# Kernel optimization log

Hardware: AMD Instinct MI355X
Metric: run time of the kernel (lower is better)

Reference implementation:

```python
import jax, jax.numpy as jnp
import numpy as np

N = 50000
E = 500000
IN_C = 100
HID = 80
OUT = 80
EDGE_DIM = 100
NUM_AGGR = 6
NUM_SCALE = 5

# PNA degree statistics, computed from the degree histogram exactly as PyG does
DEG_HIST = np.array([240, 328, 79, 39, 23, 12, 11, 7, 6, 5, 7, 3, 1, 0, 2, 0, 0, 0, 1], dtype=np.float64)
_bins = np.arange(len(DEG_HIST), dtype=np.float64)
_tot = DEG_HIST.sum()
AVG_LIN = np.float32((_bins * DEG_HIST).sum() / _tot)
AVG_LOG = np.float32((np.log(_bins + 1.0) * DEG_HIST).sum() / _tot)


def _lin_init(key, fan_in, fan_out):
    k1, k2 = jax.random.split(key)
    bound = 1.0 / np.sqrt(fan_in)
    W = jax.random.uniform(k1, (fan_in, fan_out), minval=-bound, maxval=bound, dtype=jnp.float32)
    b = jax.random.uniform(k2, (fan_out,), minval=-bound, maxval=bound, dtype=jnp.float32)
    return W, b


def setup_inputs() -> dict:
    key = jax.random.key(0)
    ks = jax.random.split(key, 20)
    inp = {}
    inp["x1"] = jax.random.normal(ks[0], (N, IN_C), jnp.float32)
    inp["edge_index1"] = jax.random.randint(ks[1], (2, E), 0, N)
    inp["edge_attr1"] = jax.random.normal(ks[2], (E, EDGE_DIM), jnp.float32)
    inp["x2"] = jax.random.normal(ks[3], (N, IN_C), jnp.float32)
    inp["edge_index2"] = jax.random.randint(ks[4], (2, E), 0, N)
    inp["edge_attr2"] = jax.random.normal(ks[5], (E, EDGE_DIM), jnp.float32)
    # conv1 params (F_in=100 -> F_out=80)
    inp["We1"], inp["be1"] = _lin_init(ks[6], EDGE_DIM, IN_C)
    inp["Wpre1"], inp["bpre1"] = _lin_init(ks[7], 3 * IN_C, IN_C)
    inp["Wpost1"], inp["bpost1"] = _lin_init(ks[8], (NUM_AGGR * NUM_SCALE + 1) * IN_C, HID)
    inp["Wlin1"], inp["blin1"] = _lin_init(ks[9], HID, HID)
    # conv2 params (F_in=80 -> F_out=80)
    inp["We2"], inp["be2"] = _lin_init(ks[10], EDGE_DIM, HID)
    inp["Wpre2"], inp["bpre2"] = _lin_init(ks[11], 3 * HID, HID)
    inp["Wpost2"], inp["bpost2"] = _lin_init(ks[12], (NUM_AGGR * NUM_SCALE + 1) * HID, OUT)
    inp["Wlin2"], inp["blin2"] = _lin_init(ks[13], OUT, OUT)
    # MLP head
    inp["Wfc1"], inp["bfc1"] = _lin_init(ks[14], OUT, 80)
    inp["Wfc2"], inp["bfc2"] = _lin_init(ks[15], 80, OUT)
    return inp


def _pna(x, src, dst, edge_attr, We, be, Wpre, bpre, Wpost, bpost, Wlin, blin):
    """PNAConv, towers=1, pre_layers=1, post_layers=1, divide_input=False."""
    F_in = x.shape[1]
    e = edge_attr @ We + be                                    # [E, F] edge encoder
    # pre_nn(cat([x_i, x_j, e])) done as 3 matmuls to avoid [E, 3F] concat
    W_i, W_j, W_e = Wpre[:F_in], Wpre[F_in:2 * F_in], Wpre[2 * F_in:]
    h = x[dst] @ W_i + x[src] @ W_j + e @ W_e + bpre           # [E, F] messages
    cnt = jax.ops.segment_sum(jnp.ones((h.shape[0],), h.dtype), dst, N)  # in-degree
    deg = jnp.maximum(cnt, 1.0)
    s = jax.ops.segment_sum(h, dst, N)                         # sum aggr
    mean = s / deg[:, None]
    mean_sq = jax.ops.segment_sum(h * h, dst, N) / deg[:, None]
    var = mean_sq - mean * mean
    std = jnp.sqrt(jnp.maximum(var, 0.0) + 1e-5)
    has = (cnt > 0)[:, None]
    mn = jnp.where(has, jax.ops.segment_min(h, dst, N), 0.0)
    mx = jnp.where(has, jax.ops.segment_max(h, dst, N), 0.0)
    agg = jnp.concatenate([s, mean, mn, mx, var, std], axis=-1)  # [N, 6F]
    logd = jnp.log(deg + 1.0)
    scaled = jnp.concatenate([
        agg,
        agg * (logd / AVG_LOG)[:, None],     # amplification
        agg * (AVG_LOG / logd)[:, None],     # attenuation
        agg * (deg / AVG_LIN)[:, None],      # linear
        agg * (AVG_LIN / deg)[:, None],      # inverse_linear
    ], axis=-1)                              # [N, 30F]
    out = jnp.concatenate([x, scaled], axis=-1) @ Wpost + bpost  # post_nn
    return out @ Wlin + blin


def _branch(x, edge_index, edge_attr, c1, c2, Wfc1, bfc1, Wfc2, bfc2):
    src, dst = edge_index[0], edge_index[1]
    x = jax.nn.relu(_pna(x, src, dst, edge_attr, *c1))
    x = _pna(x, src, dst, edge_attr, *c2)
    x = jax.nn.relu(x @ Wfc1 + bfc1)
    return x @ Wfc2 + bfc2


def reference(x1, edge_index1, edge_attr1, x2, edge_index2, edge_attr2,
              We1, be1, Wpre1, bpre1, Wpost1, bpost1, Wlin1, blin1,
              We2, be2, Wpre2, bpre2, Wpost2, bpost2, Wlin2, blin2,
              Wfc1, bfc1, Wfc2, bfc2):
    c1 = (We1, be1, Wpre1, bpre1, Wpost1, bpost1, Wlin1, blin1)
    c2 = (We2, be2, Wpre2, bpre2, Wpost2, bpost2, Wlin2, blin2)
    out1 = _branch(x1, edge_index1, edge_attr1, c1, c2, Wfc1, bfc1, Wfc2, bfc2)
    out2 = _branch(x2, edge_index2, edge_attr2, c1, c2, Wfc1, bfc1, Wfc2, bfc2)
    return (out1, out2)
```

## Files before the change

### kernel.cpp

```cpp
#include <hip/hip_runtime.h>
#include <cmath>

static constexpr int NN = 50000;
static constexpr int EE = 500000;

typedef short v8s __attribute__((ext_vector_type(8)));
typedef float v4f __attribute__((ext_vector_type(4)));

__device__ inline short f2bf(float x){
  union{float f; unsigned u;} v{x};
  unsigned r = v.u + 0x7fffu + ((v.u >> 16) & 1u);
  return (short)(r >> 16);
}
__device__ inline float b2f(short s){
  union{unsigned u; float f;} v; v.u = ((unsigned)(unsigned short)s) << 16; return v.f;
}


__global__ __launch_bounds__(256)
void count_deg_k(const int* __restrict__ dst, int* __restrict__ cnt, int e_total){
  int e = blockIdx.x*256 + threadIdx.x;
  if (e < e_total) atomicAdd(&cnt[dst[e]], 1);
}

__global__ __launch_bounds__(1024)
void scan_block_k(const int* __restrict__ cnt, int* __restrict__ pre,
                  int* __restrict__ bsum, int n){
  __shared__ int tmp[1024];
  int b = blockIdx.x, t = threadIdx.x, i = b*1024 + t;
  int v = (i < n) ? cnt[i] : 0;
  tmp[t] = v; __syncthreads();
  for (int off = 1; off < 1024; off <<= 1){
    int u = (t >= off) ? tmp[t-off] : 0;
    __syncthreads();
    tmp[t] += u;
    __syncthreads();
  }
  if (i < n) pre[i] = tmp[t];
  if (t == 1023) bsum[b] = tmp[t];
}

__global__ void scan_sums_k(int* __restrict__ bsum, int nb){
  if (threadIdx.x == 0){
    int s = 0;
    for (int i = 0; i < nb; i++){ int v = bsum[i]; bsum[i] = s; s += v; }
  }
}

__global__ __launch_bounds__(256)
void scan_finalize_k(const int* __restrict__ pre, const int* __restrict__ bsum,
                     int* __restrict__ offs, int n){
  int i = blockIdx.x*256 + threadIdx.x;
  if (i < n) offs[i+1] = pre[i] + bsum[i >> 10];
  if (i == 0) offs[0] = 0;
}

__global__ __launch_bounds__(256)
void fill_csr_k(const int* __restrict__ dst, const int* __restrict__ src,
                const int* __restrict__ offs, int* __restrict__ cursor,
                int* __restrict__ eids, int* __restrict__ srcs_csr, int e_total){
  int e = blockIdx.x*256 + threadIdx.x;
  if (e < e_total){
    int d = dst[e];
    int p = offs[d] + atomicAdd(&cursor[d], 1);
    eids[p] = e;
    srcs_csr[p] = src[e];
  }
}


__global__ __launch_bounds__(128)
void vecmat_bias_k(const float* __restrict__ v, const float* __restrict__ B,
                   const float* __restrict__ b2, float* __restrict__ out, int K, int Nc){
  int c = blockIdx.x*128 + threadIdx.x;
  if (c < Nc){
    float s = b2[c];
    for (int k = 0; k < K; k++) s += v[k]*B[(size_t)k*Nc + c];
    out[c] = s;
  }
}

__global__ __launch_bounds__(256)
void sgemm_k(const float* __restrict__ A, const float* __restrict__ B,
             float* __restrict__ C, int M, int K, int Nc){
  __shared__ float As[16][65];
  __shared__ float Bs[16][65];
  int bm = blockIdx.x*64, bn = blockIdx.y*64;
  int tid = threadIdx.x;
  int tx = tid & 15, ty = tid >> 4;
  float acc[4][4] = {};
  for (int k0 = 0; k0 < K; k0 += 16){
    #pragma unroll
    for (int i = 0; i < 4; i++){
      int t = tid + 256*i;
      int r = t >> 4, c = t & 15;
      int gr = bm + r, gc = k0 + c;
      As[c][r] = (gr < M && gc < K) ? A[(size_t)gr*K + gc] : 0.f;
    }
    #pragma unroll
    for (int i = 0; i < 4; i++){
      int t = tid + 256*i;
      int r = t >> 6, c = t & 63;
      int gr = k0 + r, gc = bn + c;
      Bs[r][c] = (gr < K && gc < Nc) ? B[(size_t)gr*Nc + gc] : 0.f;
    }
    __syncthreads();
    #pragma unroll
    for (int kk = 0; kk < 16; kk++){
      float a[4], b[4];
      #pragma unroll
      for (int i = 0; i < 4; i++) a[i] = As[kk][ty*4 + i];
      #pragma unroll
      for (int j = 0; j < 4; j++) b[j] = Bs[kk][tx*4 + j];
      #pragma unroll
      for (int i = 0; i < 4; i++)
        #pragma unroll
        for (int j = 0; j < 4; j++) acc[i][j] += a[i]*b[j];
    }
    __syncthreads();
  }
  #pragma unroll
  for (int i = 0; i < 4; i++){
    int gr = bm + ty*4 + i;
    if (gr >= M) continue;
    #pragma unroll
    for (int j = 0; j < 4; j++){
      int gc = bn + tx*4 + j;
      if (gc < Nc) C[(size_t)gr*Nc + gc] = acc[i][j];
    }
  }
}

__global__ __launch_bounds__(256)
void tconv_k(const float* __restrict__ src, int K, int ldsrc, int Ncols,
             short* __restrict__ dst, int Kpad){
  int c = blockIdx.x;
  int k = blockIdx.y*256 + threadIdx.x;
  if (c < Ncols && k < Kpad)
    dst[(long)c*Kpad + k] = (k < K) ? f2bf(src[(long)k*ldsrc + c]) : (short)0;
}

__global__ __launch_bounds__(256)
void btpost_k(const float* __restrict__ Wpost, int F, int Kpad,
              short* __restrict__ dst){
  int cp = blockIdx.x;
  int k = blockIdx.y*256 + threadIdx.x;
  if (k >= Kpad) return;
  int g = cp / 80, c = cp - g*80;
  float v = 0.f;
  if (k < F){ if (g == 0) v = Wpost[(long)k*80 + c]; }
  else if (k < 7*F) v = Wpost[(long)(F + g*6*F + (k - F))*80 + c];
  dst[(long)cp*Kpad + k] = f2bf(v);
}

__global__ __launch_bounds__(256)
void cvt_rows_k(const float* __restrict__ src, int K, short* __restrict__ dst,
                int ldd, long total){
  long i = (long)blockIdx.x*256 + threadIdx.x;
  if (i >= total) return;
  int n = (int)(i / K), c = (int)(i - (long)n*K);
  dst[(long)n*ldd + c] = f2bf(src[i]);
}

template<int NFR, bool A_F32, bool C_F32, bool RELU>
__global__ __launch_bounds__(512)
void egemm_k(const void* __restrict__ Av, long lda, int Kreal,
             const short* __restrict__ Bt, const float* __restrict__ bias,
             void* __restrict__ Cv, long ldc, int M, int ncols, int wlim)
{
  constexpr int BN = NFR*16;
  constexpr int PITCH = BN + 8;
  constexpr int NCH = 2*NFR;
  __shared__ short Bs[BN][136];
  __shared__ short stage[8*8*PITCH];
  const float* Af = (const float*)Av;
  const short* Ab = (const short*)Av;
  short* Cb = (short*)Cv;
  float* Cf = (float*)Cv;

  int bn = blockIdx.y*BN;
  for (int u = threadIdx.x; u < BN*16; u += 512){
    int c = u >> 4, k8 = (u & 15)*8;
    v8s vv = (v8s)0;
    if (bn + c < ncols) vv = *(const v8s*)(Bt + (long)(bn + c)*128 + k8);
    *(v8s*)&Bs[c][k8] = vv;
  }
  __syncthreads();

  int lane = threadIdx.x & 63;
  int lr = lane & 15, lkg = lane >> 4;
  int w = threadIdx.x >> 6;
  short* st = stage + w*8*PITCH;
  int w0 = (blockIdx.x*512 + threadIdx.x) >> 6;
  int nw = gridDim.x * 8;
  int Mtiles = (M + 31) >> 5;

  float bvs[NFR];
  #pragma unroll
  for (int n = 0; n < NFR; n++) bvs[n] = bias ? bias[bn + n*16 + lr] : 0.f;

  for (int t = w0; t < Mtiles; t += nw){
    int base = t*32;
    long r0 = base + lr;      if (r0 > M-1) r0 = M-1;
    long r1 = base + 16 + lr; if (r1 > M-1) r1 = M-1;

    v8s a0[4], a1[4];
    if constexpr (A_F32){
      const float* p0 = Af + r0*lda;
      const float* p1 = Af + r1*lda;
      #pragma unroll
      for (int ks = 0; ks < 4; ks++){
        int kb = ks*32 + lkg*8;
        v8s o0 = (v8s)0, o1 = (v8s)0;
        if (kb + 3 < Kreal){
          float4 f0 = *(const float4*)(p0 + kb);
          float4 f1 = *(const float4*)(p1 + kb);
          o0[0]=f2bf(f0.x); o0[1]=f2bf(f0.y); o0[2]=f2bf(f0.z); o0[3]=f2bf(f0.w);
          o1[0]=f2bf(f1.x); o1[1]=f2bf(f1.y); o1[2]=f2bf(f1.z); o1[3]=f2bf(f1.w);
        }
        if (kb + 7 < Kreal){
          float4 f0 = *(const float4*)(p0 + kb + 4);
          float4 f1 = *(const float4*)(p1 + kb + 4);
          o0[4]=f2bf(f0.x); o0[5]=f2bf(f0.y); o0[6]=f2bf(f0.z); o0[7]=f2bf(f0.w);
          o1[4]=f2bf(f1.x); o1[5]=f2bf(f1.y); o1[6]=f2bf(f1.z); o1[7]=f2bf(f1.w);
        }
        a0[ks] = o0; a1[ks] = o1;
      }
    } else {
      const short* p0 = Ab + r0*lda + lkg*8;
      const short* p1 = Ab + r1*lda + lkg*8;
      #pragma unroll
      for (int ks = 0; ks < 4; ks++){
        a0[ks] = *(const v8s*)(p0 + ks*32);
        a1[ks] = *(const v8s*)(p1 + ks*32);
      }
    }

    v4f acc0[NFR], acc1[NFR];
    #pragma unroll
    for (int n = 0; n < NFR; n++){ acc0[n] = (v4f)0.f; acc1[n] = (v4f)0.f; }
    #pragma unroll
    for (int ks = 0; ks < 4; ks++){
      #pragma unroll
      for (int n = 0; n < NFR; n++){
        v8s b = *(const v8s*)&Bs[n*16 + lr][ks*32 + lkg*8];
        acc0[n] = __builtin_amdgcn_mfma_f32_16x16x32_bf16(a0[ks], b, acc0[n], 0, 0, 0);
        acc1[n] = __builtin_amdgcn_mfma_f32_16x16x32_bf16(a1[ks], b, acc1[n], 0, 0, 0);
      }
    }

    if constexpr (C_F32){
      #pragma unroll
      for (int n = 0; n < NFR; n++){
        int col = bn + n*16 + lr;
        if (col >= ncols) continue;
        #pragma unroll
        for (int j = 0; j < 4; j++){
          int row = base + lkg*4 + j;
          float v0 = acc0[n][j] + bvs[n];
          float v1 = acc1[n][j] + bvs[n];
          if (RELU){ v0 = fmaxf(v0, 0.f); v1 = fmaxf(v1, 0.f); }
          if (row < M)      Cf[(long)row*ldc + col] = v0;
          if (row + 16 < M) Cf[(long)(row+16)*ldc + col] = v1;
        }
      }
    } else {
      #pragma unroll
      for (int q = 0; q < 4; q++){
        if ((lkg >> 1) == (q & 1)){
          int srow = (lkg & 1)*4;
          #pragma unroll
          for (int n = 0; n < NFR; n++){
            #pragma unroll
            for (int j = 0; j < 4; j++){
              float v = ((q < 2) ? acc0[n][j] : acc1[n][j]) + bvs[n];
              if (RELU) v = fmaxf(v, 0.f);
              st[(srow + j)*PITCH + n*16 + lr] = f2bf(v);
            }
          }
        }
        int rb = base + q*8;
        #pragma unroll
        for (int i = 0; i < (8*NCH + 63)/64; i++){
          int c = i*64 + lane;
          if (c < 8*NCH){
            int r = c/NCH, off8 = (c - r*NCH)*8;
            int grow = rb + r;
            if (grow < M && off8 < wlim - (bn & 0))
              if (bn + off8 < wlim)
                *(v8s*)(Cb + (long)grow*ldc + bn + off8) = *(const v8s*)&st[r*PITCH + off8];
          }
        }
      }
    }
  }
}

__global__ __launch_bounds__(512)
void pgemm_k(const short* __restrict__ Ab, int kpad,
             const short* __restrict__ Bt, const float* __restrict__ scl,
             const float* __restrict__ bias, short* __restrict__ C, int M)
{
  __shared__ short Bs[400][40];
  __shared__ short AsSt[10240];
  short (*As)[40] = (short(*)[40])AsSt;

  int tid = threadIdx.x;
  int w = tid >> 6, lane = tid & 63;
  int lr = lane & 15, lkg = lane >> 4;
  int bm = blockIdx.x*128;

  v4f acc[25];
  #pragma unroll
  for (int n = 0; n < 25; n++) acc[n] = (v4f)0.f;

  for (int k0 = 0; k0 < kpad; k0 += 32){
    {
      int u = tid;
      int r = u >> 2, c8 = (u & 3)*8;
      int grow = bm + r;
      v8s out = (v8s)0;
      if (grow < M) out = *(const v8s*)(Ab + (long)grow*kpad + k0 + c8);
      *(v8s*)&As[r][c8] = out;
    }
    for (int u = tid; u < 400*4; u += 512){
      int c = u >> 2, k8 = (u & 3)*8;
      *(v8s*)&Bs[c][k8] = *(const v8s*)(Bt + (long)c*kpad + k0 + k8);
    }
    __syncthreads();
    {
      v8s a = *(const v8s*)&As[w*16 + lr][lkg*8];
      #pragma unroll
      for (int n = 0; n < 25; n++){
        v8s b = *(const v8s*)&Bs[n*16 + lr][lkg*8];
        acc[n] = __builtin_amdgcn_mfma_f32_16x16x32_bf16(a, b, acc[n], 0, 0, 0);
      }
    }
    __syncthreads();
  }

  short* st = AsSt + w*16*80;
  float sc[4][5];
  #pragma unroll
  for (int j = 0; j < 4; j++){
    int row = bm + w*16 + lkg*4 + j;
    int rr = row < M ? row : 0;
    #pragma unroll
    for (int g = 0; g < 5; g++) sc[j][g] = scl[rr*5 + g];
  }
  #pragma unroll
  for (int cc = 0; cc < 5; cc++){
    float bv = bias[cc*16 + lr];
    #pragma unroll
    for (int j = 0; j < 4; j++){
      float v = bv;
      #pragma unroll
      for (int g = 0; g < 5; g++) v += sc[j][g]*acc[5*g + cc][j];
      st[(lkg*4 + j)*80 + cc*16 + lr] = f2bf(v);
    }
  }
  #pragma unroll
  for (int i = 0; i < 3; i++){
    int c = i*64 + lane;
    if (c < 160){
      int r = c/10, off = (c - r*10)*8;
      int grow = bm + w*16 + r;
      if (grow < M)
        *(v8s*)(C + (long)grow*128 + off) = *(const v8s*)&st[r*80 + off];
    }
  }
}

template<int F>
__global__ __launch_bounds__(256)
void aggregate_k(const short* __restrict__ xixj, int ldx,
                 const short* __restrict__ epc, int epoff,
                 const int* __restrict__ eids,
                 const int* __restrict__ offs, const int* __restrict__ srcs_csr,
                 short* __restrict__ aggout, long ldk,
                 float* __restrict__ scl, float avg_lin, float avg_log, int n){
  int wnode = (blockIdx.x*256 + threadIdx.x) >> 6;
  int lane = threadIdx.x & 63;
  if (wnode >= n) return;
  constexpr int C2 = F - 64;
  int beg = offs[wnode], end = offs[wnode+1];
  float xi0 = b2f(xixj[(long)wnode*ldx + lane]);
  float xi1 = (lane < C2) ? b2f(xixj[(long)wnode*ldx + 64 + lane]) : 0.f;
  float s0 = 0.f, q0 = 0.f, mn0 = INFINITY, mx0 = -INFINITY;
  float s1 = 0.f, q1 = 0.f, mn1 = INFINITY, mx1 = -INFINITY;
  for (int p = beg; p < end; p++){
    int s = srcs_csr[p];
    long e = eids[p];
    float h0 = xi0 + b2f(xixj[(long)s*ldx + F + lane]) + b2f(epc[e*192 + epoff + lane]);
    s0 += h0; q0 += h0*h0; mn0 = fminf(mn0, h0); mx0 = fmaxf(mx0, h0);
    if (lane < C2){
      float h1 = xi1 + b2f(xixj[(long)s*ldx + F + 64 + lane]) + b2f(epc[e*192 + epoff + 64 + lane]);
      s1 += h1; q1 += h1*h1; mn1 = fminf(mn1, h1); mx1 = fmaxf(mx1, h1);
    }
  }
  int cnt = end - beg;
  float deg = (float)(cnt > 1 ? cnt : 1);
  if (cnt == 0){ mn0 = 0.f; mx0 = 0.f; mn1 = 0.f; mx1 = 0.f; }
  float mean0 = s0/deg, var0 = q0/deg - mean0*mean0;
  float std0 = sqrtf(fmaxf(var0, 0.f) + 1e-5f);
  short* a = aggout + (long)wnode*ldk;
  a[lane] = f2bf(s0); a[F+lane] = f2bf(mean0); a[2*F+lane] = f2bf(mn0);
  a[3*F+lane] = f2bf(mx0); a[4*F+lane] = f2bf(var0); a[5*F+lane] = f2bf(std0);
  if (lane < C2){
    float mean1 = s1/deg, var1 = q1/deg - mean1*mean1;
    float std1 = sqrtf(fmaxf(var1, 0.f) + 1e-5f);
    int l2 = 64 + lane;
    a[l2] = f2bf(s1); a[F+l2] = f2bf(mean1); a[2*F+l2] = f2bf(mn1);
    a[3*F+l2] = f2bf(mx1); a[4*F+l2] = f2bf(var1); a[5*F+l2] = f2bf(std1);
  }
  if (lane == 0){
    float logd = logf(deg + 1.f);
    scl[wnode*5+0] = 1.f;
    scl[wnode*5+1] = logd/avg_log;
    scl[wnode*5+2] = avg_log/logd;
    scl[wnode*5+3] = deg/avg_lin;
    scl[wnode*5+4] = avg_lin/deg;
  }
}


extern "C" void kernel_launch(void* const* d_in, const int* in_sizes, int n_in,
                              void* d_out, int out_size, void* d_ws, size_t ws_size,
                              hipStream_t stream){
  const float* x1   = (const float*)d_in[0];
  const int*   ei1  = (const int*)  d_in[1];
  const float* ea1  = (const float*)d_in[2];
  const float* x2   = (const float*)d_in[3];
  const int*   ei2  = (const int*)  d_in[4];
  const float* ea2  = (const float*)d_in[5];
  const float* We1  = (const float*)d_in[6],  *be1   = (const float*)d_in[7];
  const float* Wpre1= (const float*)d_in[8],  *bpre1 = (const float*)d_in[9];
  const float* Wpost1=(const float*)d_in[10], *bpost1= (const float*)d_in[11];
  const float* Wlin1= (const float*)d_in[12], *blin1 = (const float*)d_in[13];
  const float* We2  = (const float*)d_in[14], *be2   = (const float*)d_in[15];
  const float* Wpre2= (const float*)d_in[16], *bpre2 = (const float*)d_in[17];
  const float* Wpost2=(const float*)d_in[18], *bpost2= (const float*)d_in[19];
  const float* Wlin2= (const float*)d_in[20], *blin2 = (const float*)d_in[21];
  const float* Wfc1 = (const float*)d_in[22], *bfc1  = (const float*)d_in[23];
  const float* Wfc2 = (const float*)d_in[24], *bfc2  = (const float*)d_in[25];

  static const double HIST[19] = {240,328,79,39,23,12,11,7,6,5,7,3,1,0,2,0,0,0,1};
  double tot = 0, lin = 0, lg = 0;
  for (int i = 0; i < 19; i++){ tot += HIST[i]; lin += i*HIST[i]; lg += log((double)i + 1.0)*HIST[i]; }
  float avg_lin = (float)(lin/tot), avg_log = (float)(lg/tot);

  const int KP1 = 704, KP2 = 576;

  uintptr_t pw = (uintptr_t)d_ws;
  auto carve = [&](size_t b)->void*{ void* r = (void*)pw; pw += (b + 255) & ~(size_t)255; return r; };
  int*   cnt      = (int*)  carve((size_t)NN*4);
  int*   pre      = (int*)  carve((size_t)NN*4);
  int*   bsum     = (int*)  carve(64*4);
  int*   offs     = (int*)  carve((size_t)(NN+1)*4);
  int*   cursor   = (int*)  carve((size_t)NN*4);
  int*   eids     = (int*)  carve((size_t)EE*4);
  int*   srcs_csr = (int*)  carve((size_t)EE*4);
  float* WecA     = (float*)carve(100*100*4);
  float* WecB     = (float*)carve(100*80*4);
  float* Wlf      = (float*)carve(80*80*4);
  float* becf     = (float*)carve(256*4);
  float* blf      = (float*)carve(128*4);
  short* Btep12   = (short*)carve((size_t)192*128*2);
  short* Btij1    = (short*)carve((size_t)208*128*2);
  short* Btij2    = (short*)carve((size_t)160*128*2);
  short* Btpost1  = (short*)carve((size_t)400*KP1*2);
  short* Btpost2  = (short*)carve((size_t)400*KP2*2);
  short* Btlin1   = (short*)carve((size_t)80*128*2);
  short* Btlf     = (short*)carve((size_t)80*128*2);
  short* Btfc2    = (short*)carve((size_t)80*128*2);
  short* Aprime1  = (short*)carve((size_t)NN*KP1*2);
  short* Aprime2  = (short*)carve((size_t)NN*KP2*2);
  short* xixjb    = (short*)carve((size_t)NN*224*2);
  short* epc      = (short*)carve((size_t)EE*192*2);
  float* scl      = (float*)carve((size_t)NN*5*4);
  short* tpost    = (short*)carve((size_t)NN*128*2);
  short* tD       = (short*)carve((size_t)NN*128*2);

  dim3 blk(256);
  const int NB = (NN + 1023)/1024;
  const int NTILES = (NN + 31)/32;
  const int GB_N  = (NTILES + 7)/8;
  const int GB_E  = 341;

  sgemm_k<<<dim3(2,2), blk, 0, stream>>>(We1, Wpre1 + 2*100*100, WecA, 100, 100, 100);
  sgemm_k<<<dim3(2,2), blk, 0, stream>>>(We2, Wpre2 + 2*80*80,  WecB, 100, 80, 80);
  sgemm_k<<<dim3(2,2), blk, 0, stream>>>(Wlin2, Wfc1, Wlf, 80, 80, 80);
  hipMemsetAsync(becf, 0, 256*4, stream);
  vecmat_bias_k<<<dim3(1), dim3(128), 0, stream>>>(be1, Wpre1 + 2*100*100, bpre1, becf, 100, 100);
  vecmat_bias_k<<<dim3(1), dim3(128), 0, stream>>>(be2, Wpre2 + 2*80*80,  bpre2, becf + 100, 80, 80);
  vecmat_bias_k<<<dim3(1), dim3(128), 0, stream>>>(blin2, Wfc1, bfc1, blf, 80, 80);
  tconv_k<<<dim3(100,1), blk, 0, stream>>>(WecA, 100, 100, 100, Btep12, 128);
  tconv_k<<<dim3(80,1),  blk, 0, stream>>>(WecB, 100,  80,  80, Btep12 + 100*128, 128);
  hipMemsetAsync(Btep12 + 180*128, 0, (size_t)12*128*2, stream);
  tconv_k<<<dim3(100,1), blk, 0, stream>>>(Wpre1,           100, 100, 100, Btij1,           128);
  tconv_k<<<dim3(100,1), blk, 0, stream>>>(Wpre1 + 100*100, 100, 100, 100, Btij1 + 100*128, 128);
  hipMemsetAsync(Btij1 + 200*128, 0, (size_t)8*128*2, stream);
  tconv_k<<<dim3(80,1),  blk, 0, stream>>>(Wpre2,           80, 80, 80, Btij2,          128);
  tconv_k<<<dim3(80,1),  blk, 0, stream>>>(Wpre2 + 80*80,   80, 80, 80, Btij2 + 80*128, 128);
  btpost_k<<<dim3(400,(KP1+255)/256), blk, 0, stream>>>(Wpost1, 100, KP1, Btpost1);
  btpost_k<<<dim3(400,(KP2+255)/256), blk, 0, stream>>>(Wpost2,  80, KP2, Btpost2);
  tconv_k<<<dim3(80,1), blk, 0, stream>>>(Wlin1, 80, 80, 80, Btlin1, 128);
  tconv_k<<<dim3(80,1), blk, 0, stream>>>(Wlf,   80, 80, 80, Btlf,   128);
  tconv_k<<<dim3(80,1), blk, 0, stream>>>(Wfc2,  80, 80, 80, Btfc2,  128);
  hipMemsetAsync(Aprime1, 0, (size_t)NN*KP1*2, stream);
  hipMemsetAsync(Aprime2, 0, (size_t)NN*KP2*2, stream);
  hipMemsetAsync(tpost,   0, (size_t)NN*128*2, stream);
  hipMemsetAsync(tD,      0, (size_t)NN*128*2, stream);

  for (int b = 0; b < 2; b++){
    const float* x  = b ? x2  : x1;
    const int*   ei = b ? ei2 : ei1;
    const float* ea = b ? ea2 : ea1;
    float* outb = (float*)d_out + (size_t)b*NN*80;
    const int* src = ei;
    const int* dst = ei + EE;

    hipMemsetAsync(cnt, 0, (size_t)NN*4, stream);
    hipMemsetAsync(cursor, 0, (size_t)NN*4, stream);
    count_deg_k<<<dim3((EE+255)/256), blk, 0, stream>>>(dst, cnt, EE);
    scan_block_k<<<dim3(NB), dim3(1024), 0, stream>>>(cnt, pre, bsum, NN);
    scan_sums_k<<<dim3(1), dim3(64), 0, stream>>>(bsum, NB);
    scan_finalize_k<<<dim3((NN+255)/256), blk, 0, stream>>>(pre, bsum, offs, NN);
    fill_csr_k<<<dim3((EE+255)/256), blk, 0, stream>>>(dst, src, offs, cursor, eids, srcs_csr, EE);

    egemm_k<4,true,false,false><<<dim3(GB_E,3), dim3(512), 0, stream>>>(
        ea, 100, 100, Btep12, becf, epc, 192, EE, 180, 192);

    cvt_rows_k<<<dim3((int)(((long)NN*100 + 255)/256)), blk, 0, stream>>>(x, 100, Aprime1, KP1, (long)NN*100);

    egemm_k<5,false,false,false><<<dim3(GB_N,3), dim3(512), 0, stream>>>(
        Aprime1, KP1, 0, Btij1, nullptr, xixjb, 224, NN, 200, 200);
    aggregate_k<100><<<dim3((NN+3)/4), blk, 0, stream>>>(
        xixjb, 224, epc, 0, eids, offs, srcs_csr, Aprime1 + 100, KP1, scl, avg_lin, avg_log, NN);
    pgemm_k<<<dim3((NN+127)/128), dim3(512), 0, stream>>>(
        Aprime1, KP1, Btpost1, scl, bpost1, tpost, NN);
    egemm_k<5,false,false,true><<<dim3(GB_N,1), dim3(512), 0, stream>>>(
        tpost, 128, 0, Btlin1, blin1, Aprime2, KP2, NN, 80, 80);

    egemm_k<5,false,false,false><<<dim3(GB_N,2), dim3(512), 0, stream>>>(
        Aprime2, KP2, 0, Btij2, nullptr, xixjb, 160, NN, 160, 160);
    aggregate_k<80><<<dim3((NN+3)/4), blk, 0, stream>>>(
        xixjb, 160, epc, 100, eids, offs, srcs_csr, Aprime2 + 80, KP2, scl, avg_lin, avg_log, NN);
    pgemm_k<<<dim3((NN+127)/128), dim3(512), 0, stream>>>(
        Aprime2, KP2, Btpost2, scl, bpost2, tpost, NN);

    egemm_k<5,false,false,true><<<dim3(GB_N,1), dim3(512), 0, stream>>>(
        tpost, 128, 0, Btlf, blf, tD, 128, NN, 80, 80);
    egemm_k<5,false,true,false><<<dim3(GB_N,1), dim3(512), 0, stream>>>(
        tD, 128, 0, Btfc2, bfc2, outb, 80, NN, 80, 80);
  }
}
```

Measured before the change: 1.497 ms.

## Batch setup kernels, pack CSR edges, shrink GEMM blocks, use packed bf16 convert

Several small prep launches (vecmat, tconv, memsets) are merged into multi-job kernels, and the full-buffer memsets become a pad-only zeroing kernel. The CSR edge id and source arrays are packed into one int2 array, so aggregation does a single load per edge. egemm blocks drop from 512 to 256 threads with new grid sizes, and the edge GEMM moves to 6 fragments over 2 column blocks. The fp32 A path loads all values first and converts them with the hardware packed bf16 instruction. The goal is less launch overhead and better memory-level parallelism, at the cost of possible occupancy and rounding-behaviour differences.

Result: faster. 1.322 ms (-11.7%).

```diff
diff --git a/kernel.cpp b/kernel.cpp
--- a/kernel.cpp
+++ b/kernel.cpp
@@ -14,6 +14,11 @@
 }
 __device__ inline float b2f(short s){
   union{unsigned u; float f;} v; v.u = ((unsigned)(unsigned short)s) << 16; return v.f;
+}
+__device__ inline unsigned cvtpk(float lo, float hi){
+  unsigned r;
+  asm("v_cvt_pk_bf16_f32 %0, %1, %2" : "=v"(r) : "v"(lo), "v"(hi));
+  return r;
 }
 
 
@@ -58,25 +63,26 @@
 __global__ __launch_bounds__(256)
 void fill_csr_k(const int* __restrict__ dst, const int* __restrict__ src,
                 const int* __restrict__ offs, int* __restrict__ cursor,
-                int* __restrict__ eids, int* __restrict__ srcs_csr, int e_total){
+                int2* __restrict__ edg, int e_total){
   int e = blockIdx.x*256 + threadIdx.x;
   if (e < e_total){
     int d = dst[e];
     int p = offs[d] + atomicAdd(&cursor[d], 1);
-    eids[p] = e;
-    srcs_csr[p] = src[e];
-  }
-}
-
-
+    edg[p] = make_int2(e, src[e]);
+  }
+}
+
+
+struct VJob { const float* v; const float* B; const float* b2; float* out; int K, Nc; };
+struct VJobs { VJob j[3]; };
 __global__ __launch_bounds__(128)
-void vecmat_bias_k(const float* __restrict__ v, const float* __restrict__ B,
-                   const float* __restrict__ b2, float* __restrict__ out, int K, int Nc){
-  int c = blockIdx.x*128 + threadIdx.x;
-  if (c < Nc){
-    float s = b2[c];
-    for (int k = 0; k < K; k++) s += v[k]*B[(size_t)k*Nc + c];
-    out[c] = s;
+void vecmat_multi_k(VJobs js){
+  const VJob J = js.j[blockIdx.y];
+  int c = threadIdx.x;
+  if (c < J.Nc){
+    float s = J.b2[c];
+    for (int k = 0; k < J.K; k++) s += J.v[k]*J.B[(size_t)k*J.Nc + c];
+    J.out[c] = s;
   }
 }
 
@@ -131,13 +137,15 @@
   }
 }
 
-__global__ __launch_bounds__(256)
-void tconv_k(const float* __restrict__ src, int K, int ldsrc, int Ncols,
-             short* __restrict__ dst, int Kpad){
+struct TJob { const float* src; short* dst; int K, ldsrc, Ncols; };
+struct TJobs { TJob j[9]; };
+__global__ __launch_bounds__(128)
+void tconv_multi_k(TJobs js){
+  const TJob J = js.j[blockIdx.y];
   int c = blockIdx.x;
-  int k = blockIdx.y*256 + threadIdx.x;
-  if (c < Ncols && k < Kpad)
-    dst[(long)c*Kpad + k] = (k < K) ? f2bf(src[(long)k*ldsrc + c]) : (short)0;
+  int k = threadIdx.x;
+  if (c < J.Ncols)
+    J.dst[(long)c*128 + k] = (k < J.K) ? f2bf(J.src[(long)k*J.ldsrc + c]) : (short)0;
 }
 
 __global__ __launch_bounds__(256)
@@ -162,8 +170,18 @@
   dst[(long)n*ldd + c] = f2bf(src[i]);
 }
 
+struct ZJob { short* p; int ld, c0, nc, rows; };
+struct ZJobs { ZJob j[4]; };
+__global__ __launch_bounds__(256)
+void zeropad_k(ZJobs js){
+  const ZJob J = js.j[blockIdx.y];
+  int i = blockIdx.x*256 + threadIdx.x;
+  int r = i / J.nc, c = i - r*J.nc;
+  if (r < J.rows) J.p[(long)r*J.ld + J.c0 + c] = 0;
+}
+
 template<int NFR, bool A_F32, bool C_F32, bool RELU>
-__global__ __launch_bounds__(512)
+__global__ __launch_bounds__(256)
 void egemm_k(const void* __restrict__ Av, long lda, int Kreal,
              const short* __restrict__ Bt, const float* __restrict__ bias,
              void* __restrict__ Cv, long ldc, int M, int ncols, int wlim)
@@ -172,14 +190,14 @@
   constexpr int PITCH = BN + 8;
   constexpr int NCH = 2*NFR;
   __shared__ short Bs[BN][136];
-  __shared__ short stage[8*8*PITCH];
+  __shared__ short stage[4*8*PITCH];
   const float* Af = (const float*)Av;
   const short* Ab = (const short*)Av;
   short* Cb = (short*)Cv;
   float* Cf = (float*)Cv;
 
   int bn = blockIdx.y*BN;
-  for (int u = threadIdx.x; u < BN*16; u += 512){
+  for (int u = threadIdx.x; u < BN*16; u += 256){
     int c = u >> 4, k8 = (u & 15)*8;
     v8s vv = (v8s)0;
     if (bn + c < ncols) vv = *(const v8s*)(Bt + (long)(bn + c)*128 + k8);
@@ -191,8 +209,8 @@
   int lr = lane & 15, lkg = lane >> 4;
   int w = threadIdx.x >> 6;
   short* st = stage + w*8*PITCH;
-  int w0 = (blockIdx.x*512 + threadIdx.x) >> 6;
-  int nw = gridDim.x * 8;
+  int w0 = (blockIdx.x*256 + threadIdx.x) >> 6;
+  int nw = gridDim.x * 4;
   int Mtiles = (M + 31) >> 5;
 
   float bvs[NFR];
@@ -208,23 +226,28 @@
     if constexpr (A_F32){
       const float* p0 = Af + r0*lda;
       const float* p1 = Af + r1*lda;
+      float4 f0[8], f1[8];
       #pragma unroll
       for (int ks = 0; ks < 4; ks++){
         int kb = ks*32 + lkg*8;
-        v8s o0 = (v8s)0, o1 = (v8s)0;
-        if (kb + 3 < Kreal){
-          float4 f0 = *(const float4*)(p0 + kb);
-          float4 f1 = *(const float4*)(p1 + kb);
-          o0[0]=f2bf(f0.x); o0[1]=f2bf(f0.y); o0[2]=f2bf(f0.z); o0[3]=f2bf(f0.w);
-          o1[0]=f2bf(f1.x); o1[1]=f2bf(f1.y); o1[2]=f2bf(f1.z); o1[3]=f2bf(f1.w);
-        }
-        if (kb + 7 < Kreal){
-          float4 f0 = *(const float4*)(p0 + kb + 4);
-          float4 f1 = *(const float4*)(p1 + kb + 4);
-          o0[4]=f2bf(f0.x); o0[5]=f2bf(f0.y); o0[6]=f2bf(f0.z); o0[7]=f2bf(f0.w);
-          o1[4]=f2bf(f1.x); o1[5]=f2bf(f1.y); o1[6]=f2bf(f1.z); o1[7]=f2bf(f1.w);
-        }
-        a0[ks] = o0; a1[ks] = o1;
+        bool ok0 = (kb + 3 < Kreal), ok1 = (kb + 7 < Kreal);
+        f0[ks*2+0] = ok0 ? *(const float4*)(p0 + kb)     : make_float4(0.f,0.f,0.f,0.f);
+        f0[ks*2+1] = ok1 ? *(const float4*)(p0 + kb + 4) : make_float4(0.f,0.f,0.f,0.f);
+        f1[ks*2+0] = ok0 ? *(const float4*)(p1 + kb)     : make_float4(0.f,0.f,0.f,0.f);
+        f1[ks*2+1] = ok1 ? *(const float4*)(p1 + kb + 4) : make_float4(0.f,0.f,0.f,0.f);
+      }
+      #pragma unroll
+      for (int ks = 0; ks < 4; ks++){
+        union { v8s s; unsigned u[4]; } o0, o1;
+        o0.u[0] = cvtpk(f0[ks*2].x, f0[ks*2].y);
+        o0.u[1] = cvtpk(f0[ks*2].z, f0[ks*2].w);
+        o0.u[2] = cvtpk(f0[ks*2+1].x, f0[ks*2+1].y);
+        o0.u[3] = cvtpk(f0[ks*2+1].z, f0[ks*2+1].w);
+        o1.u[0] = cvtpk(f1[ks*2].x, f1[ks*2].y);
+        o1.u[1] = cvtpk(f1[ks*2].z, f1[ks*2].w);
+        o1.u[2] = cvtpk(f1[ks*2+1].x, f1[ks*2+1].y);
+        o1.u[3] = cvtpk(f1[ks*2+1].z, f1[ks*2+1].w);
+        a0[ks] = o0.s; a1[ks] = o1.s;
       }
     } else {
       const short* p0 = Ab + r0*lda + lkg*8;
@@ -286,9 +309,8 @@
           if (c < 8*NCH){
             int r = c/NCH, off8 = (c - r*NCH)*8;
             int grow = rb + r;
-            if (grow < M && off8 < wlim - (bn & 0))
-              if (bn + off8 < wlim)
-                *(v8s*)(Cb + (long)grow*ldc + bn + off8) = *(const v8s*)&st[r*PITCH + off8];
+            if (grow < M && bn + off8 < wlim)
+              *(v8s*)(Cb + (long)grow*ldc + bn + off8) = *(const v8s*)&st[r*PITCH + off8];
           }
         }
       }
@@ -375,8 +397,8 @@
 __global__ __launch_bounds__(256)
 void aggregate_k(const short* __restrict__ xixj, int ldx,
                  const short* __restrict__ epc, int epoff,
-                 const int* __restrict__ eids,
-                 const int* __restrict__ offs, const int* __restrict__ srcs_csr,
+                 const int2* __restrict__ edg,
+                 const int* __restrict__ offs,
                  short* __restrict__ aggout, long ldk,
                  float* __restrict__ scl, float avg_lin, float avg_log, int n){
   int wnode = (blockIdx.x*256 + threadIdx.x) >> 6;
@@ -389,8 +411,8 @@
   float s0 = 0.f, q0 = 0.f, mn0 = INFINITY, mx0 = -INFINITY;
   float s1 = 0.f, q1 = 0.f, mn1 = INFINITY, mx1 = -INFINITY;
   for (int p = beg; p < end; p++){
-    int s = srcs_csr[p];
-    long e = eids[p];
+    int2 es = edg[p];
+    long e = es.x; int s = es.y;
     float h0 = xi0 + b2f(xixj[(long)s*ldx + F + lane]) + b2f(epc[e*192 + epoff + lane]);
     s0 += h0; q0 += h0*h0; mn0 = fminf(mn0, h0); mx0 = fmaxf(mx0, h0);
     if (lane < C2){
@@ -454,12 +476,11 @@
   uintptr_t pw = (uintptr_t)d_ws;
   auto carve = [&](size_t b)->void*{ void* r = (void*)pw; pw += (b + 255) & ~(size_t)255; return r; };
   int*   cnt      = (int*)  carve((size_t)NN*4);
+  int*   cursor   = (int*)  carve((size_t)NN*4);
   int*   pre      = (int*)  carve((size_t)NN*4);
   int*   bsum     = (int*)  carve(64*4);
   int*   offs     = (int*)  carve((size_t)(NN+1)*4);
-  int*   cursor   = (int*)  carve((size_t)NN*4);
-  int*   eids     = (int*)  carve((size_t)EE*4);
-  int*   srcs_csr = (int*)  carve((size_t)EE*4);
+  int2*  edg      = (int2*) carve((size_t)EE*8);
   float* WecA     = (float*)carve(100*100*4);
   float* WecB     = (float*)carve(100*80*4);
   float* Wlf      = (float*)carve(80*80*4);
@@ -483,34 +504,43 @@
 
   dim3 blk(256);
   const int NB = (NN + 1023)/1024;
-  const int NTILES = (NN + 31)/32;
-  const int GB_N  = (NTILES + 7)/8;
-  const int GB_E  = 341;
+  const int GB_N = 391;
+  const int GB_E = 1024;
 
   sgemm_k<<<dim3(2,2), blk, 0, stream>>>(We1, Wpre1 + 2*100*100, WecA, 100, 100, 100);
   sgemm_k<<<dim3(2,2), blk, 0, stream>>>(We2, Wpre2 + 2*80*80,  WecB, 100, 80, 80);
   sgemm_k<<<dim3(2,2), blk, 0, stream>>>(Wlin2, Wfc1, Wlf, 80, 80, 80);
   hipMemsetAsync(becf, 0, 256*4, stream);
-  vecmat_bias_k<<<dim3(1), dim3(128), 0, stream>>>(be1, Wpre1 + 2*100*100, bpre1, becf, 100, 100);
-  vecmat_bias_k<<<dim3(1), dim3(128), 0, stream>>>(be2, Wpre2 + 2*80*80,  bpre2, becf + 100, 80, 80);
-  vecmat_bias_k<<<dim3(1), dim3(128), 0, stream>>>(blin2, Wfc1, bfc1, blf, 80, 80);
-  tconv_k<<<dim3(100,1), blk, 0, stream>>>(WecA, 100, 100, 100, Btep12, 128);
-  tconv_k<<<dim3(80,1),  blk, 0, stream>>>(WecB, 100,  80,  80, Btep12 + 100*128, 128);
-  hipMemsetAsync(Btep12 + 180*128, 0, (size_t)12*128*2, stream);
-  tconv_k<<<dim3(100,1), blk, 0, stream>>>(Wpre1,           100, 100, 100, Btij1,           128);
-  tconv_k<<<dim3(100,1), blk, 0, stream>>>(Wpre1 + 100*100, 100, 100, 100, Btij1 + 100*128, 128);
-  hipMemsetAsync(Btij1 + 200*128, 0, (size_t)8*128*2, stream);
-  tconv_k<<<dim3(80,1),  blk, 0, stream>>>(Wpre2,           80, 80, 80, Btij2,          128);
-  tconv_k<<<dim3(80,1),  blk, 0, stream>>>(Wpre2 + 80*80,   80, 80, 80, Btij2 + 80*128, 128);
+  {
+    VJobs vj;
+    vj.j[0] = {be1,  Wpre1 + 2*100*100, bpre1, becf,       100, 100};
+    vj.j[1] = {be2,  Wpre2 + 2*80*80,   bpre2, becf + 100,  80,  80};
+    vj.j[2] = {blin2, Wfc1,             bfc1,  blf,         80,  80};
+    vecmat_multi_k<<<dim3(1,3), dim3(128), 0, stream>>>(vj);
+  }
+  {
+    TJobs tj;
+    tj.j[0] = {WecA,            Btep12,            100, 100, 100};
+    tj.j[1] = {WecB,            Btep12 + 100*128,  100,  80,  80};
+    tj.j[2] = {Wpre1,           Btij1,             100, 100, 100};
+    tj.j[3] = {Wpre1 + 100*100, Btij1 + 100*128,   100, 100, 100};
+    tj.j[4] = {Wpre2,           Btij2,              80,  80,  80};
+    tj.j[5] = {Wpre2 + 80*80,   Btij2 + 80*128,     80,  80,  80};
+    tj.j[6] = {Wlin1,           Btlin1,             80,  80,  80};
+    tj.j[7] = {Wlf,             Btlf,               80,  80,  80};
+    tj.j[8] = {Wfc2,            Btfc2,              80,  80,  80};
+    tconv_multi_k<<<dim3(100,9), dim3(128), 0, stream>>>(tj);
+  }
   btpost_k<<<dim3(400,(KP1+255)/256), blk, 0, stream>>>(Wpost1, 100, KP1, Btpost1);
   btpost_k<<<dim3(400,(KP2+255)/256), blk, 0, stream>>>(Wpost2,  80, KP2, Btpost2);
-  tconv_k<<<dim3(80,1), blk, 0, stream>>>(Wlin1, 80, 80, 80, Btlin1, 128);
-  tconv_k<<<dim3(80,1), blk, 0, stream>>>(Wlf,   80, 80, 80, Btlf,   128);
-  tconv_k<<<dim3(80,1), blk, 0, stream>>>(Wfc2,  80, 80, 80, Btfc2,  128);
-  hipMemsetAsync(Aprime1, 0, (size_t)NN*KP1*2, stream);
-  hipMemsetAsync(Aprime2, 0, (size_t)NN*KP2*2, stream);
-  hipMemsetAsync(tpost,   0, (size_t)NN*128*2, stream);
-  hipMemsetAsync(tD,      0, (size_t)NN*128*2, stream);
+  {
+    ZJobs zj;
+    zj.j[0] = {Aprime1, KP1, 700,  4, NN};
+    zj.j[1] = {Aprime2, KP2, 560, 16, NN};
+    zj.j[2] = {tpost,   128,  80, 48, NN};
+    zj.j[3] = {tD,      128,  80, 48, NN};
+    zeropad_k<<<dim3((NN*48 + 255)/256, 4), blk, 0, stream>>>(zj);
+  }
 
   for (int b = 0; b < 2; b++){
     const float* x  = b ? x2  : x1;
@@ -520,38 +550,37 @@
     const int* src = ei;
     const int* dst = ei + EE;
 
-    hipMemsetAsync(cnt, 0, (size_t)NN*4, stream);
-    hipMemsetAsync(cursor, 0, (size_t)NN*4, stream);
+    hipMemsetAsync(cnt, 0, (uintptr_t)pre - (uintptr_t)cnt, stream);
     count_deg_k<<<dim3((EE+255)/256), blk, 0, stream>>>(dst, cnt, EE);
     scan_block_k<<<dim3(NB), dim3(1024), 0, stream>>>(cnt, pre, bsum, NN);
     scan_sums_k<<<dim3(1), dim3(64), 0, stream>>>(bsum, NB);
     scan_finalize_k<<<dim3((NN+255)/256), blk, 0, stream>>>(pre, bsum, offs, NN);
-    fill_csr_k<<<dim3((EE+255)/256), blk, 0, stream>>>(dst, src, offs, cursor, eids, srcs_csr, EE);
-
-    egemm_k<4,true,false,false><<<dim3(GB_E,3), dim3(512), 0, stream>>>(
+    fill_csr_k<<<dim3((EE+255)/256), blk, 0, stream>>>(dst, src, offs, cursor, edg, EE);
+
+    egemm_k<6,true,false,false><<<dim3(GB_E,2), blk, 0, stream>>>(
         ea, 100, 100, Btep12, becf, epc, 192, EE, 180, 192);
 
     cvt_rows_k<<<dim3((int)(((long)NN*100 + 255)/256)), blk, 0, stream>>>(x, 100, Aprime1, KP1, (long)NN*100);
 
-    egemm_k<5,false,false,false><<<dim3(GB_N,3), dim3(512), 0, stream>>>(
+    egemm_k<5,false,false,false><<<dim3(GB_N,3), blk, 0, stream>>>(
         Aprime1, KP1, 0, Btij1, nullptr, xixjb, 224, NN, 200, 200);
     aggregate_k<100><<<dim3((NN+3)/4), blk, 0, stream>>>(
-        xixjb, 224, epc, 0, eids, offs, srcs_csr, Aprime1 + 100, KP1, scl, avg_lin, avg_log, NN);
+        xixjb, 224, epc, 0, edg, offs, Aprime1 + 100, KP1, scl, avg_lin, avg_log, NN);
     pgemm_k<<<dim3((NN+127)/128), dim3(512), 0, stream>>>(
         Aprime1, KP1, Btpost1, scl, bpost1, tpost, NN);
-    egemm_k<5,false,false,true><<<dim3(GB_N,1), dim3(512), 0, stream>>>(
+    egemm_k<5,false,false,true><<<dim3(GB_N,1), blk, 0, stream>>>(
         tpost, 128, 0, Btlin1, blin1, Aprime2, KP2, NN, 80, 80);
 
-    egemm_k<5,false,false,false><<<dim3(GB_N,2), dim3(512), 0, stream>>>(
+    egemm_k<5,false,false,false><<<dim3(GB_N,2), blk, 0, stream>>>(
         Aprime2, KP2, 0, Btij2, nullptr, xixjb, 160, NN, 160, 160);
     aggregate_k<80><<<dim3((NN+3)/4), blk, 0, stream>>>(
-        xixjb, 160, epc, 100, eids, offs, srcs_csr, Aprime2 + 80, KP2, scl, avg_lin, avg_log, NN);
+        xixjb, 160, epc, 100, edg, offs, Aprime2 + 80, KP2, scl, avg_lin, avg_log, NN);
     pgemm_k<<<dim3((NN+127)/128), dim3(512), 0, stream>>>(
         Aprime2, KP2, Btpost2, scl, bpost2, tpost, NN);
 
-    egemm_k<5,false,false,true><<<dim3(GB_N,1), dim3(512), 0, stream>>>(
+    egemm_k<5,false,false,true><<<dim3(GB_N,1), blk, 0, stream>>>(
         tpost, 128, 0, Btlf, blf, tD, 128, NN, 80, 80);
-    egemm_k<5,false,true,false><<<dim3(GB_N,1), dim3(512), 0, stream>>>(
+    egemm_k<5,false,true,false><<<dim3(GB_N,1), blk, 0, stream>>>(
         tD, 128, 0, Btfc2, bfc2, outb, 80, NN, 80, 80);
   }
 }
```
